# Optimization experiments

Hardware: AMD Instinct MI355X
Metric: run time of the kernel (lower is better)

Reference implementation:

```python
import jax, jax.numpy as jnp
import numpy as np

N_NODES = 10000
N_EDGES = 20000
N_GRAPHS = 64
DIM = 64
NFEAT = 32
EDIM = 16
NCLS = 10
EPS = 1e-5  # BatchNorm eps (torch default)


def setup_inputs() -> dict:
    key = jax.random.key(0)
    ks = jax.random.split(key, 20)
    def w(k, shape, s=0.05):
        return jax.random.normal(k, shape, dtype=jnp.float32) * s
    z = lambda *s: jnp.zeros(s, jnp.float32)
    inp = {}
    inp["x"] = jax.random.normal(ks[0], (N_NODES, NFEAT), dtype=jnp.float32)
    inp["edge_index"] = jax.random.randint(ks[1], (2, N_EDGES), 0, N_NODES)
    inp["edge_attr"] = jax.random.normal(ks[2], (N_EDGES, EDIM), dtype=jnp.float32)
    inp["batch"] = jax.random.randint(ks[3], (N_NODES,), 0, N_GRAPHS)
    # edge_transform
    inp["et_w"] = w(ks[4], (EDIM, DIM)); inp["et_b"] = z(DIM)
    # conv_in edge-MLP (dim->128->num_features*dim) + root weight + bias
    inp["nn1_w1"] = w(ks[5], (DIM, 128)); inp["nn1_b1"] = z(128)
    inp["nn1_w2"] = w(ks[6], (128, NFEAT * DIM)); inp["nn1_b2"] = z(NFEAT * DIM)
    inp["root_in"] = w(ks[7], (NFEAT, DIM)); inp["bias_in"] = z(DIM)
    # 4 residual NNConv layers, params stacked on leading axis
    inp["convs_w1"] = w(ks[8], (4, DIM, 128)); inp["convs_b1"] = z(4, 128)
    inp["convs_w2"] = w(ks[9], (4, 128, DIM * DIM)); inp["convs_b2"] = z(4, DIM * DIM)
    inp["convs_root"] = w(ks[10], (4, DIM, DIM)); inp["convs_bias"] = z(4, DIM)
    # 5 BatchNorm layers (affine)
    inp["bn_gamma"] = jnp.ones((5, DIM), jnp.float32); inp["bn_beta"] = z(5, DIM)
    # head
    inp["lin1_w"] = w(ks[11], (DIM, DIM)); inp["lin1_b"] = z(DIM)
    inp["lin2_w"] = w(ks[12], (DIM, DIM)); inp["lin2_b"] = z(DIM)
    inp["lout_w"] = w(ks[13], (DIM, NCLS)); inp["lout_b"] = z(NCLS)
    return inp


def _bn(x, g, b):
    # BatchNorm1d training-mode math: biased variance over nodes
    m = x.mean(0)
    v = jnp.mean((x - m) ** 2, 0)
    return g * (x - m) / jnp.sqrt(v + EPS) + b


def _nnconv(x, src, dst, e, w1, b1, w2, b2, root, bias, in_dim):
    # PyG NNConv: per-edge weight matrix from edge MLP, gather->bmm->scatter-add, plus root transform
    h = jax.nn.relu(e @ w1 + b1)                       # [E,128]
    W = (h @ w2 + b2).reshape(-1, in_dim, DIM)         # [E,in,out]
    msg = jnp.einsum('ei,eio->eo', x[src], W)          # [E,out]
    agg = jax.ops.segment_sum(msg, dst, num_segments=N_NODES)
    return agg + x @ root + bias


def reference(x, edge_index, edge_attr, batch,
              et_w, et_b,
              nn1_w1, nn1_b1, nn1_w2, nn1_b2, root_in, bias_in,
              convs_w1, convs_b1, convs_w2, convs_b2, convs_root, convs_bias,
              bn_gamma, bn_beta,
              lin1_w, lin1_b, lin2_w, lin2_b, lout_w, lout_b):
    src, dst = edge_index[0], edge_index[1]
    e = edge_attr @ et_w + et_b                        # [E,DIM]
    h = jax.nn.relu(_bn(
        _nnconv(x, src, dst, e, nn1_w1, nn1_b1, nn1_w2, nn1_b2, root_in, bias_in, NFEAT),
        bn_gamma[0], bn_beta[0]))
    for k in range(4):  # residual NNConv blocks
        h = jax.nn.relu(_bn(
            _nnconv(h, src, dst, e, convs_w1[k], convs_b1[k], convs_w2[k], convs_b2[k],
                    convs_root[k], convs_bias[k], DIM),
            bn_gamma[k + 1], bn_beta[k + 1])) + h
    g = jax.ops.segment_max(h, batch, num_segments=N_GRAPHS)  # global_max_pool
    g = jax.nn.relu(g @ lin1_w + lin1_b)  # dropout = identity (eval/deterministic)
    g = jax.nn.relu(g @ lin2_w + lin2_b)
    return jax.nn.sigmoid(g @ lout_w + lout_b)
```

## Files before the change

### kernel.cpp

```cpp
#include <hip/hip_runtime.h>
#include <hip/hip_bf16.h>
#include <math.h>

#define N_NODES 10000
#define N_EDGES 20000
#define EPAD 20224
#define N_GRAPHS 64
#define DIM 64
#define NFEAT 32
#define EDIM 16
#define NCLS 10

typedef short short8 __attribute__((ext_vector_type(8)));
typedef float f32x16 __attribute__((ext_vector_type(16)));

static __device__ __forceinline__ short f2b(float f) {
  __hip_bfloat16 h = __float2bfloat16(f);
  return __builtin_bit_cast(short, h);
}

static __device__ __forceinline__ void gload_lds16(const void* g, void* s) {
  __builtin_amdgcn_global_load_lds(
      (const __attribute__((address_space(1))) unsigned int*)g,
      (__attribute__((address_space(3))) unsigned int*)s, 16, 0, 0);
}

__global__ __launch_bounds__(256) void k_pack_all(
    const float* __restrict__ w20, const float* __restrict__ b20,
    const float* __restrict__ w2c, const float* __restrict__ b2c,
    short* __restrict__ pk, float* __restrict__ gpool) {
  const int b = blockIdx.x, t = threadIdx.x;
  if (b == 0) { for (int i = t; i < N_GRAPHS * DIM; i += 256) gpool[i] = 0.f; }
  __shared__ float tile[32][65];
  const float *w2, *b2; short* out; int K, lb;
  if (b < 129) { w2 = w20; b2 = b20; out = pk; K = 4096; lb = b; }
  else {
    int bb = b - 129; int k = bb / 258; lb = bb % 258;
    w2 = w2c + (size_t)k * 8192 * 64; b2 = b2c + (size_t)k * 4096;
    out = pk + 264192 + (size_t)k * 528384; K = 8192;
  }
  #pragma unroll
  for (int it = 0; it < 2; ++it) {
    int idx = t + it * 256;
    int r = idx >> 4, c4 = idx & 15;
    int k = lb * 32 + r;
    const float* sp = (k < K) ? (w2 + (size_t)k * 64 + c4 * 4)
                              : (b2 + (size_t)(k - K) * 64 + c4 * 4);
    float4 v = *(const float4*)sp;
    float* dr = &tile[r][c4 * 4];
    dr[0] = v.x; dr[1] = v.y; dr[2] = v.z; dr[3] = v.w;
  }
  __syncthreads();
  const int S_local = t >> 7, n = (t >> 6) & 1, l = t & 63;
  const int rbase = S_local * 16 + ((l >> 5) << 3);
  const int col = n * 32 + (l & 31);
  short8 o;
  #pragma unroll
  for (int u = 0; u < 8; ++u) o[u] = f2b(tile[rbase + u][col]);
  ((short8*)out)[(size_t)lb * 256 + t] = o;
}

__global__ __launch_bounds__(256) void k_ef_mlp1(
    const float* __restrict__ ea, const float* __restrict__ etw,
    const float* __restrict__ etb, const float* __restrict__ w1,
    const float* __restrict__ b1, float* __restrict__ e_feat,
    float* __restrict__ h1) {
  __shared__ float sea[8][17];
  __shared__ float se[8][65];
  const int b = blockIdx.x, t = threadIdx.x;
  const int e0 = b * 8;
  if (t < 128) {
    int r = t >> 4, c = t & 15;
    sea[r][c] = ea[(size_t)(e0 + r) * EDIM + c];
  }
  __syncthreads();
  {
    int o = t & 63, eh = t >> 6;
    #pragma unroll
    for (int k = 0; k < 2; ++k) {
      int r = eh * 2 + k;
      float a = etb[o];
      #pragma unroll
      for (int i = 0; i < EDIM; ++i) a = fmaf(sea[r][i], etw[i * 64 + o], a);
      se[r][o] = a;
      e_feat[(size_t)(e0 + r) * 64 + o] = a;
    }
  }
  __syncthreads();
  {
    int j = t & 127, eh = t >> 7;
    int r0 = eh * 4;
    float a0 = b1[j], a1 = a0, a2 = a0, a3 = a0;
    #pragma unroll 8
    for (int i = 0; i < 64; ++i) {
      float wv = w1[i * 128 + j];
      a0 = fmaf(se[r0 + 0][i], wv, a0);
      a1 = fmaf(se[r0 + 1][i], wv, a1);
      a2 = fmaf(se[r0 + 2][i], wv, a2);
      a3 = fmaf(se[r0 + 3][i], wv, a3);
    }
    size_t base = (size_t)(e0 + r0) * 128 + j;
    h1[base +   0] = fmaxf(a0, 0.f);
    h1[base + 128] = fmaxf(a1, 0.f);
    h1[base + 256] = fmaxf(a2, 0.f);
    h1[base + 384] = fmaxf(a3, 0.f);
  }
}

__global__ __launch_bounds__(256) void k_root0(const float* __restrict__ x,
    const float* __restrict__ rootw, const float* __restrict__ rootb,
    float* __restrict__ agg, double* __restrict__ part0) {
  if (blockIdx.x == 0 && threadIdx.x < 128) part0[threadIdx.x] = 0.0;
  int idx = blockIdx.x * 256 + threadIdx.x;
  if (idx >= N_NODES * DIM) return;
  int n = idx >> 6, o = idx & 63;
  float a = rootb[o];
  const float* hr = x + (size_t)n * NFEAT;
  #pragma unroll 8
  for (int i = 0; i < NFEAT; ++i) a = fmaf(hr[i], rootw[i * 64 + o], a);
  agg[idx] = a;
}

template<int IN>
__global__ __launch_bounds__(256, 2) void k_msg(
    const float* __restrict__ h1, const float* __restrict__ xin,
    const int* __restrict__ src, const short* __restrict__ pk,
    float* __restrict__ pt) {
  constexpr int QW = IN / 16;
  constexpr int JR = 32;
  constexpr int GBYTES = QW * 2048;
  __shared__ float sh_h[256][JR + 1];
  __shared__ __align__(16) short bbuf[2][QW * 1024];
  const int t = threadIdx.x, l = t & 63, w = t >> 6;
  const int e0 = blockIdx.x * 256;
  const int jbase = blockIdx.y * JR;
  const int ng = JR + (blockIdx.y == 0 ? 1 : 0);

  const char* pkc = (const char*)pk;
  const char* bias_gb = pkc + (size_t)(8 * IN) * 2048;

  auto stage = [&](int g) {
    const char* gb = (g < JR) ? pkc + (size_t)(jbase + g) * GBYTES : bias_gb;
    #pragma unroll
    for (int s = 0; s < QW / 2; ++s) {
      int off = w * (GBYTES / 4) + s * 1024;
      gload_lds16(gb + off + l * 16, (char*)&bbuf[g & 1][0] + off);
    }
  };

  #pragma unroll
  for (int it = 0; it < 8; ++it) {
    int idx = t + it * 256;
    int row = idx >> 3, c4 = idx & 7;
    int e = e0 + row;
    float4 v = {0.f, 0.f, 0.f, 0.f};
    if (e < N_EDGES) v = *(const float4*)(h1 + (size_t)e * 128 + jbase + c4 * 4);
    float* dr = &sh_h[row][c4 * 4];
    dr[0] = v.x; dr[1] = v.y; dr[2] = v.z; dr[3] = v.w;
  }
  stage(0);

  const int h8 = (l >> 5) << 3;
  float xr[2][QW][8];
  #pragma unroll
  for (int m = 0; m < 2; ++m) {
    int eme = e0 + w * 64 + m * 32 + (l & 31);
    int srow = src[eme < N_EDGES ? eme : 0];
    #pragma unroll
    for (int q = 0; q < QW; ++q) {
      const float* xp = xin + (size_t)srow * IN + q * 16 + h8;
      float4 a = *(const float4*)xp;
      float4 bq = *(const float4*)(xp + 4);
      xr[m][q][0] = a.x;  xr[m][q][1] = a.y;  xr[m][q][2] = a.z;  xr[m][q][3] = a.w;
      xr[m][q][4] = bq.x; xr[m][q][5] = bq.y; xr[m][q][6] = bq.z; xr[m][q][7] = bq.w;
    }
  }

  f32x16 acc00 = {}, acc01 = {}, acc10 = {}, acc11 = {};

  for (int g = 0; g < ng; ++g) {
    asm volatile("s_waitcnt vmcnt(0)" ::: "memory");
    __syncthreads();
    if (g + 1 < ng) stage(g + 1);
    const short8* bp = (const short8*)&bbuf[g & 1][0];
    if (g < JR) {
      float hv0 = sh_h[w * 64 + (l & 31)][g];
      float hv1 = sh_h[w * 64 + 32 + (l & 31)][g];
      #pragma unroll
      for (int q = 0; q < QW; ++q) {
        short8 b0 = bp[q * 128 + l];
        short8 b1 = bp[q * 128 + 64 + l];
        short8 av0, av1;
        #pragma unroll
        for (int u = 0; u < 8; ++u) {
          av0[u] = f2b(hv0 * xr[0][q][u]);
          av1[u] = f2b(hv1 * xr[1][q][u]);
        }
        acc00 = __builtin_amdgcn_mfma_f32_32x32x16_bf16(av0, b0, acc00, 0, 0, 0);
        acc01 = __builtin_amdgcn_mfma_f32_32x32x16_bf16(av0, b1, acc01, 0, 0, 0);
        acc10 = __builtin_amdgcn_mfma_f32_32x32x16_bf16(av1, b0, acc10, 0, 0, 0);
        acc11 = __builtin_amdgcn_mfma_f32_32x32x16_bf16(av1, b1, acc11, 0, 0, 0);
      }
    } else {
      #pragma unroll
      for (int q = 0; q < QW; ++q) {
        short8 b0 = bp[q * 128 + l];
        short8 b1 = bp[q * 128 + 64 + l];
        short8 av0, av1;
        #pragma unroll
        for (int u = 0; u < 8; ++u) {
          av0[u] = f2b(xr[0][q][u]);
          av1[u] = f2b(xr[1][q][u]);
        }
        acc00 = __builtin_amdgcn_mfma_f32_32x32x16_bf16(av0, b0, acc00, 0, 0, 0);
        acc01 = __builtin_amdgcn_mfma_f32_32x32x16_bf16(av0, b1, acc01, 0, 0, 0);
        acc10 = __builtin_amdgcn_mfma_f32_32x32x16_bf16(av1, b0, acc10, 0, 0, 0);
        acc11 = __builtin_amdgcn_mfma_f32_32x32x16_bf16(av1, b1, acc11, 0, 0, 0);
      }
    }
  }

  float* po = pt + ((size_t)blockIdx.y * EPAD + e0 + w * 64) * 64 + (l & 31);
  #pragma unroll
  for (int v = 0; v < 16; ++v) {
    int r = (v & 3) + ((v >> 2) << 3) + ((l >> 5) << 2);
    po[(size_t)r * 64]             = acc00[v];
    po[(size_t)r * 64 + 32]       = acc01[v];
    po[(size_t)(r + 32) * 64]      = acc10[v];
    po[(size_t)(r + 32) * 64 + 32] = acc11[v];
  }
}

__global__ __launch_bounds__(256) void k_reduce(const float* __restrict__ pt,
    const int* __restrict__ dst, float* __restrict__ agg) {
  int idx = blockIdx.x * 256 + threadIdx.x;
  int e = idx >> 4;
  if (e >= N_EDGES) return;
  int c = (idx & 15) * 4;
  const float* p = pt + (size_t)e * 64 + c;
  float4 s0 = *(const float4*)p;
  float4 s1 = *(const float4*)(p + (size_t)EPAD * 64);
  float4 s2 = *(const float4*)(p + (size_t)2 * EPAD * 64);
  float4 s3 = *(const float4*)(p + (size_t)3 * EPAD * 64);
  float* ap = agg + (size_t)dst[e] * 64 + c;
  atomicAdd(ap + 0, s0.x + s1.x + s2.x + s3.x);
  atomicAdd(ap + 1, s0.y + s1.y + s2.y + s3.y);
  atomicAdd(ap + 2, s0.z + s1.z + s2.z + s3.z);
  atomicAdd(ap + 3, s0.w + s1.w + s2.w + s3.w);
}

__global__ __launch_bounds__(256) void k_bnpart(const float* __restrict__ agg,
    double* __restrict__ part) {
  const int t = threadIdx.x;
  const int c = t & 63, rg = t >> 6;
  const int r0 = blockIdx.x * 50;
  const int r1 = min(r0 + 50, N_NODES);
  double s = 0.0, s2 = 0.0;
  for (int r = r0 + rg; r < r1; r += 4) {
    float v = agg[(size_t)r * 64 + c];
    s += v;
    s2 += (double)v * v;
  }
  __shared__ double shs[4][64];
  __shared__ double shq[4][64];
  shs[rg][c] = s; shq[rg][c] = s2;
  __syncthreads();
  if (t < 64) {
    double ts = shs[0][t] + shs[1][t] + shs[2][t] + shs[3][t];
    double tq = shq[0][t] + shq[1][t] + shq[2][t] + shq[3][t];
    atomicAdd(&part[t], ts);
    atomicAdd(&part[64 + t], tq);
  }
}

__global__ __launch_bounds__(256) void k_inter(
    const float* __restrict__ agg, const double* __restrict__ part,
    const float* __restrict__ gamma, const float* __restrict__ beta,
    const float* resid, float* __restrict__ hout,
    const float* __restrict__ rootw, const float* __restrict__ rootb,
    float* __restrict__ aggn, double* __restrict__ partn,
    const float* __restrict__ ef, const float* __restrict__ w1,
    const float* __restrict__ b1, float* __restrict__ h1) {
  const int b = blockIdx.x, t = threadIdx.x;
  if (b < 157) {
    __shared__ float sh[64][65];
    if (b == 0 && t < 128) partn[t] = 0.0;
    const int o = t & 63, rg = t >> 6;
    const int n0 = b * 64;
    float m = (float)(part[o] * (1.0 / N_NODES));
    float s2 = (float)(part[64 + o] * (1.0 / N_NODES));
    float inv = 1.0f / sqrtf(s2 - m * m + 1e-5f);
    float sc = gamma[o] * inv;
    float sf = beta[o] - m * sc;
    #pragma unroll
    for (int k = 0; k < 16; ++k) {
      int r = rg * 16 + k;
      int n = n0 + r;
      float v = 0.f;
      if (n < N_NODES) {
        v = fmaxf(fmaf(agg[(size_t)n * 64 + o], sc, sf), 0.f);
        if (resid) v += resid[(size_t)n * 64 + o];
        hout[(size_t)n * 64 + o] = v;
      }
      sh[r][o] = v;
    }
    __syncthreads();
    float acc[16];
    float rb = rootb[o];
    #pragma unroll
    for (int k = 0; k < 16; ++k) acc[k] = rb;
    for (int i = 0; i < 64; ++i) {
      float wv = rootw[i * 64 + o];
      #pragma unroll
      for (int k = 0; k < 16; ++k) acc[k] = fmaf(sh[rg * 16 + k][i], wv, acc[k]);
    }
    #pragma unroll
    for (int k = 0; k < 16; ++k) {
      int n = n0 + rg * 16 + k;
      if (n < N_NODES) aggn[(size_t)n * 64 + o] = acc[k];
    }
  } else {
    const int e0 = (b - 157) * 8;
    __shared__ float se[8][65];
    {
      int r = t >> 5, ci = (t & 31) * 2;
      const float* sp = ef + (size_t)(e0 + r) * 64 + ci;
      se[r][ci] = sp[0];
      se[r][ci + 1] = sp[1];
    }
    __syncthreads();
    const int j = t & 127, eh = t >> 7;
    const int r0 = eh * 4;
    float a0 = b1[j], a1 = a0, a2 = a0, a3 = a0;
    #pragma unroll 8
    for (int i = 0; i < 64; ++i) {
      float wv = w1[i * 128 + j];
      a0 = fmaf(se[r0 + 0][i], wv, a0);
      a1 = fmaf(se[r0 + 1][i], wv, a1);
      a2 = fmaf(se[r0 + 2][i], wv, a2);
      a3 = fmaf(se[r0 + 3][i], wv, a3);
    }
    size_t base = (size_t)(e0 + r0) * 128 + j;
    h1[base +   0] = fmaxf(a0, 0.f);
    h1[base + 128] = fmaxf(a1, 0.f);
    h1[base + 256] = fmaxf(a2, 0.f);
    h1[base + 384] = fmaxf(a3, 0.f);
  }
}

__global__ __launch_bounds__(256) void k_final(const float* __restrict__ agg,
    const double* __restrict__ part, const float* __restrict__ gamma,
    const float* __restrict__ beta, const float* __restrict__ resid,
    const int* __restrict__ batch, float* __restrict__ gpool) {
  int idx = blockIdx.x * 256 + threadIdx.x;
  if (idx >= N_NODES * DIM) return;
  int c = idx & 63, r = idx >> 6;
  float m = (float)(part[c] * (1.0 / N_NODES));
  float s2 = (float)(part[64 + c] * (1.0 / N_NODES));
  float inv = 1.0f / sqrtf(s2 - m * m + 1e-5f);
  float sc = gamma[c] * inv;
  float sf = beta[c] - m * sc;
  float v = fmaxf(fmaf(agg[idx], sc, sf), 0.f) + resid[idx];
  atomicMax((unsigned int*)&gpool[batch[r] * 64 + c], __float_as_uint(v));
}

__global__ __launch_bounds__(64) void k_head(const float* __restrict__ g,
    const float* __restrict__ w1, const float* __restrict__ b1,
    const float* __restrict__ w2, const float* __restrict__ b2,
    const float* __restrict__ wo, const float* __restrict__ bo,
    float* __restrict__ out) {
  __shared__ float s0[64];
  __shared__ float s1[64];
  const int r = blockIdx.x, t = threadIdx.x;
  s0[t] = g[r * 64 + t];
  __syncthreads();
  float a = b1[t];
  #pragma unroll 8
  for (int i = 0; i < 64; ++i) a = fmaf(s0[i], w1[i * 64 + t], a);
  s1[t] = fmaxf(a, 0.f);
  __syncthreads();
  a = b2[t];
  #pragma unroll 8
  for (int i = 0; i < 64; ++i) a = fmaf(s1[i], w2[i * 64 + t], a);
  __syncthreads();
  s0[t] = fmaxf(a, 0.f);
  __syncthreads();
  if (t < NCLS) {
    float o = bo[t];
    #pragma unroll 8
    for (int i = 0; i < 64; ++i) o = fmaf(s0[i], wo[i * NCLS + t], o);
    out[r * NCLS + t] = 1.f / (1.f + expf(-o));
  }
}

extern "C" void kernel_launch(void* const* d_in, const int* in_sizes, int n_in,
                              void* d_out, int out_size, void* d_ws, size_t ws_size,
                              hipStream_t stream) {
  const float* x          = (const float*)d_in[0];
  const int*   eidx       = (const int*)d_in[1];
  const float* eattr      = (const float*)d_in[2];
  const int*   batch      = (const int*)d_in[3];
  const float* et_w       = (const float*)d_in[4];
  const float* et_b       = (const float*)d_in[5];
  const float* nn1_w1     = (const float*)d_in[6];
  const float* nn1_b1     = (const float*)d_in[7];
  const float* nn1_w2     = (const float*)d_in[8];
  const float* nn1_b2     = (const float*)d_in[9];
  const float* root_in    = (const float*)d_in[10];
  const float* bias_in    = (const float*)d_in[11];
  const float* convs_w1   = (const float*)d_in[12];
  const float* convs_b1   = (const float*)d_in[13];
  const float* convs_w2   = (const float*)d_in[14];
  const float* convs_b2   = (const float*)d_in[15];
  const float* convs_root = (const float*)d_in[16];
  const float* convs_bias = (const float*)d_in[17];
  const float* bn_gamma   = (const float*)d_in[18];
  const float* bn_beta    = (const float*)d_in[19];
  const float* lin1_w     = (const float*)d_in[20];
  const float* lin1_b     = (const float*)d_in[21];
  const float* lin2_w     = (const float*)d_in[22];
  const float* lin2_b     = (const float*)d_in[23];
  const float* lout_w     = (const float*)d_in[24];
  const float* lout_b     = (const float*)d_in[25];

  const int* srcp = eidx;
  const int* dstp = eidx + N_EDGES;

  double* part0 = (double*)d_ws;
  double* part1 = part0 + 128;
  float* e_feat = (float*)(part0 + 256);
  float* h1     = e_feat + N_EDGES * DIM;
  float* agg    = h1 + N_EDGES * 128;
  float* h_cur  = agg + N_NODES * DIM;
  float* g      = h_cur + N_NODES * DIM;
  short* pk0    = (short*)(g + N_GRAPHS * DIM);
  short* pkL[4];
  for (int k = 0; k < 4; ++k) pkL[k] = pk0 + 264192 + (size_t)k * 528384;
  float* pt     = (float*)(pk0 + 264192 + 4 * 528384);
  double* parts[2] = {part0, part1};

  const dim3 gMsg(79, 4);
  const int gRed = EPAD * 16 / 256;

  k_pack_all<<<1161, 256, 0, stream>>>(nn1_w2, nn1_b2, convs_w2, convs_b2, pk0, g);
  k_ef_mlp1<<<2500, 256, 0, stream>>>(eattr, et_w, et_b, nn1_w1, nn1_b1,
                                      e_feat, h1);
  k_root0<<<2500, 256, 0, stream>>>(x, root_in, bias_in, agg, part0);

  k_msg<NFEAT><<<gMsg, 256, 0, stream>>>(h1, x, srcp, pk0, pt);
  k_reduce<<<gRed, 256, 0, stream>>>(pt, dstp, agg);
  k_bnpart<<<200, 256, 0, stream>>>(agg, part0);

  for (int k = 0; k < 4; ++k) {
    k_inter<<<2657, 256, 0, stream>>>(
        agg, parts[k & 1], bn_gamma + k * 64, bn_beta + k * 64,
        (k == 0) ? nullptr : h_cur, h_cur,
        convs_root + (size_t)k * 4096, convs_bias + (size_t)k * 64,
        agg, parts[(k + 1) & 1],
        e_feat, convs_w1 + (size_t)k * 64 * 128, convs_b1 + (size_t)k * 128, h1);
    k_msg<DIM><<<gMsg, 256, 0, stream>>>(h1, h_cur, srcp, pkL[k], pt);
    k_reduce<<<gRed, 256, 0, stream>>>(pt, dstp, agg);
    k_bnpart<<<200, 256, 0, stream>>>(agg, parts[(k + 1) & 1]);
  }

  k_final<<<2500, 256, 0, stream>>>(agg, parts[0], bn_gamma + 4 * 64,
                                    bn_beta + 4 * 64, h_cur, batch, g);
  k_head<<<N_GRAPHS, 64, 0, stream>>>(g, lin1_w, lin1_b, lin2_w, lin2_b,
                                      lout_w, lout_b, (float*)d_out);
}
```

Measured before the change: 444.6 us.

## Fuse edge reduction into message kernel and split hidden units across waves

The message kernel is restructured so that each block owns 64 edges and its four waves split the 128 hidden units, 32 each. Weight fragments are now read straight from global memory into registers with double buffering, replacing the LDS staging. The per-wave partial results are summed in LDS and scattered to nodes with atomics inside the same kernel. This removes the separate reduce kernel and the large partial-sum buffer, and the edge-MLP output is stored transposed so per-edge hidden values load coalesced. In exchange, every block re-reads the whole packed weight matrix from global or L2 memory instead of sharing a staged copy, and register pressure rises.

```diff
diff --git a/kernel.cpp b/kernel.cpp
--- a/kernel.cpp
+++ b/kernel.cpp
@@ -17,12 +17,6 @@
 static __device__ __forceinline__ short f2b(float f) {
   __hip_bfloat16 h = __float2bfloat16(f);
   return __builtin_bit_cast(short, h);
-}
-
-static __device__ __forceinline__ void gload_lds16(const void* g, void* s) {
-  __builtin_amdgcn_global_load_lds(
-      (const __attribute__((address_space(1))) unsigned int*)g,
-      (__attribute__((address_space(3))) unsigned int*)s, 16, 0, 0);
 }
 
 __global__ __launch_bounds__(256) void k_pack_all(
@@ -64,7 +58,7 @@
     const float* __restrict__ ea, const float* __restrict__ etw,
     const float* __restrict__ etb, const float* __restrict__ w1,
     const float* __restrict__ b1, float* __restrict__ e_feat,
-    float* __restrict__ h1) {
+    float* __restrict__ h1T) {
   __shared__ float sea[8][17];
   __shared__ float se[8][65];
   const int b = blockIdx.x, t = threadIdx.x;
@@ -99,11 +93,8 @@
       a2 = fmaf(se[r0 + 2][i], wv, a2);
       a3 = fmaf(se[r0 + 3][i], wv, a3);
     }
-    size_t base = (size_t)(e0 + r0) * 128 + j;
-    h1[base +   0] = fmaxf(a0, 0.f);
-    h1[base + 128] = fmaxf(a1, 0.f);
-    h1[base + 256] = fmaxf(a2, 0.f);
-    h1[base + 384] = fmaxf(a3, 0.f);
+    float4 o = {fmaxf(a0, 0.f), fmaxf(a1, 0.f), fmaxf(a2, 0.f), fmaxf(a3, 0.f)};
+    *(float4*)(h1T + (size_t)j * EPAD + e0 + r0) = o;
   }
 }
 
@@ -123,48 +114,23 @@
 
 template<int IN>
 __global__ __launch_bounds__(256, 2) void k_msg(
-    const float* __restrict__ h1, const float* __restrict__ xin,
-    const int* __restrict__ src, const short* __restrict__ pk,
-    float* __restrict__ pt) {
+    const float* __restrict__ h1T, const float* __restrict__ xin,
+    const int* __restrict__ src, const int* __restrict__ dst,
+    const short* __restrict__ pk, float* __restrict__ agg) {
   constexpr int QW = IN / 16;
   constexpr int JR = 32;
-  constexpr int GBYTES = QW * 2048;
-  __shared__ float sh_h[256][JR + 1];
-  __shared__ __align__(16) short bbuf[2][QW * 1024];
+  __shared__ float red[4][64][68];
   const int t = threadIdx.x, l = t & 63, w = t >> 6;
-  const int e0 = blockIdx.x * 256;
-  const int jbase = blockIdx.y * JR;
-  const int ng = JR + (blockIdx.y == 0 ? 1 : 0);
-
-  const char* pkc = (const char*)pk;
-  const char* bias_gb = pkc + (size_t)(8 * IN) * 2048;
-
-  auto stage = [&](int g) {
-    const char* gb = (g < JR) ? pkc + (size_t)(jbase + g) * GBYTES : bias_gb;
-    #pragma unroll
-    for (int s = 0; s < QW / 2; ++s) {
-      int off = w * (GBYTES / 4) + s * 1024;
-      gload_lds16(gb + off + l * 16, (char*)&bbuf[g & 1][0] + off);
-    }
-  };
-
-  #pragma unroll
-  for (int it = 0; it < 8; ++it) {
-    int idx = t + it * 256;
-    int row = idx >> 3, c4 = idx & 7;
-    int e = e0 + row;
-    float4 v = {0.f, 0.f, 0.f, 0.f};
-    if (e < N_EDGES) v = *(const float4*)(h1 + (size_t)e * 128 + jbase + c4 * 4);
-    float* dr = &sh_h[row][c4 * 4];
-    dr[0] = v.x; dr[1] = v.y; dr[2] = v.z; dr[3] = v.w;
-  }
-  stage(0);
-
+  const int e0 = blockIdx.x * 64;
+  const int jbase = w * JR;
+  const int col = l & 31;
   const int h8 = (l >> 5) << 3;
+  const short8* B = (const short8*)pk;
+
   float xr[2][QW][8];
   #pragma unroll
   for (int m = 0; m < 2; ++m) {
-    int eme = e0 + w * 64 + m * 32 + (l & 31);
+    int eme = e0 + m * 32 + col;
     int srow = src[eme < N_EDGES ? eme : 0];
     #pragma unroll
     for (int q = 0; q < QW; ++q) {
@@ -178,75 +144,87 @@
 
   f32x16 acc00 = {}, acc01 = {}, acc10 = {}, acc11 = {};
 
-  for (int g = 0; g < ng; ++g) {
-    asm volatile("s_waitcnt vmcnt(0)" ::: "memory");
-    __syncthreads();
-    if (g + 1 < ng) stage(g + 1);
-    const short8* bp = (const short8*)&bbuf[g & 1][0];
-    if (g < JR) {
-      float hv0 = sh_h[w * 64 + (l & 31)][g];
-      float hv1 = sh_h[w * 64 + 32 + (l & 31)][g];
+  short8 bufA[QW * 2], bufB[QW * 2];
+  float2 hA, hB;
+
+#define LOADB(buf, j)                                              \
+  { int S0_ = (j) * QW;                                            \
+    _Pragma("unroll")                                              \
+    for (int q = 0; q < QW; ++q) {                                 \
+      buf[q * 2]     = B[(size_t)(S0_ + q) * 128 + l];             \
+      buf[q * 2 + 1] = B[(size_t)(S0_ + q) * 128 + 64 + l];        \
+    } }
+#define LOADH(hv, j)                                               \
+  { hv.x = h1T[(size_t)(j) * EPAD + e0 + col];                     \
+    hv.y = h1T[(size_t)(j) * EPAD + e0 + 32 + col]; }
+#define COMPUTE(buf, hv)                                           \
+  { _Pragma("unroll")                                              \
+    for (int q = 0; q < QW; ++q) {                                 \
+      short8 av0, av1;                                             \
+      _Pragma("unroll")                                            \
+      for (int u = 0; u < 8; ++u) {                                \
+        av0[u] = f2b(hv.x * xr[0][q][u]);                          \
+        av1[u] = f2b(hv.y * xr[1][q][u]);                          \
+      }                                                            \
+      acc00 = __builtin_amdgcn_mfma_f32_32x32x16_bf16(av0, buf[q*2],   acc00, 0, 0, 0); \
+      acc01 = __builtin_amdgcn_mfma_f32_32x32x16_bf16(av0, buf[q*2+1], acc01, 0, 0, 0); \
+      acc10 = __builtin_amdgcn_mfma_f32_32x32x16_bf16(av1, buf[q*2],   acc10, 0, 0, 0); \
+      acc11 = __builtin_amdgcn_mfma_f32_32x32x16_bf16(av1, buf[q*2+1], acc11, 0, 0, 0); \
+    } }
+
+  LOADB(bufA, jbase); LOADH(hA, jbase);
+  for (int g = 0; g < JR; g += 2) {
+    LOADB(bufB, jbase + g + 1); LOADH(hB, jbase + g + 1);
+    COMPUTE(bufA, hA);
+    if (g + 2 < JR) { LOADB(bufA, jbase + g + 2); LOADH(hA, jbase + g + 2); }
+    COMPUTE(bufB, hB);
+  }
+  if (w == 0) {
+    LOADB(bufA, 128);
+    #pragma unroll
+    for (int q = 0; q < QW; ++q) {
+      short8 av0, av1;
       #pragma unroll
-      for (int q = 0; q < QW; ++q) {
-        short8 b0 = bp[q * 128 + l];
-        short8 b1 = bp[q * 128 + 64 + l];
-        short8 av0, av1;
-        #pragma unroll
-        for (int u = 0; u < 8; ++u) {
-          av0[u] = f2b(hv0 * xr[0][q][u]);
-          av1[u] = f2b(hv1 * xr[1][q][u]);
-        }
-        acc00 = __builtin_amdgcn_mfma_f32_32x32x16_bf16(av0, b0, acc00, 0, 0, 0);
-        acc01 = __builtin_amdgcn_mfma_f32_32x32x16_bf16(av0, b1, acc01, 0, 0, 0);
-        acc10 = __builtin_amdgcn_mfma_f32_32x32x16_bf16(av1, b0, acc10, 0, 0, 0);
-        acc11 = __builtin_amdgcn_mfma_f32_32x32x16_bf16(av1, b1, acc11, 0, 0, 0);
+      for (int u = 0; u < 8; ++u) {
+        av0[u] = f2b(xr[0][q][u]);
+        av1[u] = f2b(xr[1][q][u]);
       }
-    } else {
-      #pragma unroll
-      for (int q = 0; q < QW; ++q) {
-        short8 b0 = bp[q * 128 + l];
-        short8 b1 = bp[q * 128 + 64 + l];
-        short8 av0, av1;
-        #pragma unroll
-        for (int u = 0; u < 8; ++u) {
-          av0[u] = f2b(xr[0][q][u]);
-          av1[u] = f2b(xr[1][q][u]);
-        }
-        acc00 = __builtin_amdgcn_mfma_f32_32x32x16_bf16(av0, b0, acc00, 0, 0, 0);
-        acc01 = __builtin_amdgcn_mfma_f32_32x32x16_bf16(av0, b1, acc01, 0, 0, 0);
-        acc10 = __builtin_amdgcn_mfma_f32_32x32x16_bf16(av1, b0, acc10, 0, 0, 0);
-        acc11 = __builtin_amdgcn_mfma_f32_32x32x16_bf16(av1, b1, acc11, 0, 0, 0);
-      }
-    }
-  }
-
-  float* po = pt + ((size_t)blockIdx.y * EPAD + e0 + w * 64) * 64 + (l & 31);
+      acc00 = __builtin_amdgcn_mfma_f32_32x32x16_bf16(av0, bufA[q*2],   acc00, 0, 0, 0);
+      acc01 = __builtin_amdgcn_mfma_f32_32x32x16_bf16(av0, bufA[q*2+1], acc01, 0, 0, 0);
+      acc10 = __builtin_amdgcn_mfma_f32_32x32x16_bf16(av1, bufA[q*2],   acc10, 0, 0, 0);
+      acc11 = __builtin_amdgcn_mfma_f32_32x32x16_bf16(av1, bufA[q*2+1], acc11, 0, 0, 0);
+    }
+  }
+#undef LOADB
+#undef LOADH
+#undef COMPUTE
+
   #pragma unroll
   for (int v = 0; v < 16; ++v) {
     int r = (v & 3) + ((v >> 2) << 3) + ((l >> 5) << 2);
-    po[(size_t)r * 64]             = acc00[v];
-    po[(size_t)r * 64 + 32]       = acc01[v];
-    po[(size_t)(r + 32) * 64]      = acc10[v];
-    po[(size_t)(r + 32) * 64 + 32] = acc11[v];
-  }
-}
-
-__global__ __launch_bounds__(256) void k_reduce(const float* __restrict__ pt,
-    const int* __restrict__ dst, float* __restrict__ agg) {
-  int idx = blockIdx.x * 256 + threadIdx.x;
-  int e = idx >> 4;
-  if (e >= N_EDGES) return;
-  int c = (idx & 15) * 4;
-  const float* p = pt + (size_t)e * 64 + c;
-  float4 s0 = *(const float4*)p;
-  float4 s1 = *(const float4*)(p + (size_t)EPAD * 64);
-  float4 s2 = *(const float4*)(p + (size_t)2 * EPAD * 64);
-  float4 s3 = *(const float4*)(p + (size_t)3 * EPAD * 64);
-  float* ap = agg + (size_t)dst[e] * 64 + c;
-  atomicAdd(ap + 0, s0.x + s1.x + s2.x + s3.x);
-  atomicAdd(ap + 1, s0.y + s1.y + s2.y + s3.y);
-  atomicAdd(ap + 2, s0.z + s1.z + s2.z + s3.z);
-  atomicAdd(ap + 3, s0.w + s1.w + s2.w + s3.w);
+    red[w][r][col]           = acc00[v];
+    red[w][r][col + 32]      = acc01[v];
+    red[w][r + 32][col]      = acc10[v];
+    red[w][r + 32][col + 32] = acc11[v];
+  }
+  __syncthreads();
+
+  const int row = t >> 2, cq = (t & 3) * 16;
+  const int e = e0 + row;
+  if (e < N_EDGES) {
+    float* ap = agg + (size_t)dst[e] * 64 + cq;
+    #pragma unroll
+    for (int cc = 0; cc < 4; ++cc) {
+      float4 s0 = *(const float4*)&red[0][row][cq + cc * 4];
+      float4 s1 = *(const float4*)&red[1][row][cq + cc * 4];
+      float4 s2 = *(const float4*)&red[2][row][cq + cc * 4];
+      float4 s3 = *(const float4*)&red[3][row][cq + cc * 4];
+      atomicAdd(ap + cc * 4 + 0, s0.x + s1.x + s2.x + s3.x);
+      atomicAdd(ap + cc * 4 + 1, s0.y + s1.y + s2.y + s3.y);
+      atomicAdd(ap + cc * 4 + 2, s0.z + s1.z + s2.z + s3.z);
+      atomicAdd(ap + cc * 4 + 3, s0.w + s1.w + s2.w + s3.w);
+    }
+  }
 }
 
 __global__ __launch_bounds__(256) void k_bnpart(const float* __restrict__ agg,
@@ -280,7 +258,7 @@
     const float* __restrict__ rootw, const float* __restrict__ rootb,
     float* __restrict__ aggn, double* __restrict__ partn,
     const float* __restrict__ ef, const float* __restrict__ w1,
-    const float* __restrict__ b1, float* __restrict__ h1) {
+    const float* __restrict__ b1, float* __restrict__ h1T) {
   const int b = blockIdx.x, t = threadIdx.x;
   if (b < 157) {
     __shared__ float sh[64][65];
@@ -340,11 +318,8 @@
       a2 = fmaf(se[r0 + 2][i], wv, a2);
       a3 = fmaf(se[r0 + 3][i], wv, a3);
     }
-    size_t base = (size_t)(e0 + r0) * 128 + j;
-    h1[base +   0] = fmaxf(a0, 0.f);
-    h1[base + 128] = fmaxf(a1, 0.f);
-    h1[base + 256] = fmaxf(a2, 0.f);
-    h1[base + 384] = fmaxf(a3, 0.f);
+    float4 o = {fmaxf(a0, 0.f), fmaxf(a1, 0.f), fmaxf(a2, 0.f), fmaxf(a3, 0.f)};
+    *(float4*)(h1T + (size_t)j * EPAD + e0 + r0) = o;
   }
 }
 
@@ -429,26 +404,23 @@
   double* part0 = (double*)d_ws;
   double* part1 = part0 + 128;
   float* e_feat = (float*)(part0 + 256);
-  float* h1     = e_feat + N_EDGES * DIM;
-  float* agg    = h1 + N_EDGES * 128;
+  float* h1T    = e_feat + N_EDGES * DIM;
+  float* agg    = h1T + 128 * EPAD;
   float* h_cur  = agg + N_NODES * DIM;
   float* g      = h_cur + N_NODES * DIM;
   short* pk0    = (short*)(g + N_GRAPHS * DIM);
   short* pkL[4];
   for (int k = 0; k < 4; ++k) pkL[k] = pk0 + 264192 + (size_t)k * 528384;
-  float* pt     = (float*)(pk0 + 264192 + 4 * 528384);
   double* parts[2] = {part0, part1};
 
-  const dim3 gMsg(79, 4);
-  const int gRed = EPAD * 16 / 256;
+  const int gMsg = (N_EDGES + 63) / 64;
 
   k_pack_all<<<1161, 256, 0, stream>>>(nn1_w2, nn1_b2, convs_w2, convs_b2, pk0, g);
   k_ef_mlp1<<<2500, 256, 0, stream>>>(eattr, et_w, et_b, nn1_w1, nn1_b1,
-                                      e_feat, h1);
+                                      e_feat, h1T);
   k_root0<<<2500, 256, 0, stream>>>(x, root_in, bias_in, agg, part0);
 
-  k_msg<NFEAT><<<gMsg, 256, 0, stream>>>(h1, x, srcp, pk0, pt);
-  k_reduce<<<gRed, 256, 0, stream>>>(pt, dstp, agg);
+  k_msg<NFEAT><<<gMsg, 256, 0, stream>>>(h1T, x, srcp, dstp, pk0, agg);
   k_bnpart<<<200, 256, 0, stream>>>(agg, part0);
 
   for (int k = 0; k < 4; ++k) {
@@ -457,9 +429,8 @@
         (k == 0) ? nullptr : h_cur, h_cur,
         convs_root + (size_t)k * 4096, convs_bias + (size_t)k * 64,
         agg, parts[(k + 1) & 1],
-        e_feat, convs_w1 + (size_t)k * 64 * 128, convs_b1 + (size_t)k * 128, h1);
-    k_msg<DIM><<<gMsg, 256, 0, stream>>>(h1, h_cur, srcp, pkL[k], pt);
-    k_reduce<<<gRed, 256, 0, stream>>>(pt, dstp, agg);
+        e_feat, convs_w1 + (size_t)k * 64 * 128, convs_b1 + (size_t)k * 128, h1T);
+    k_msg<DIM><<<gMsg, 256, 0, stream>>>(h1T, h_cur, srcp, dstp, pkL[k], agg);
     k_bnpart<<<200, 256, 0, stream>>>(agg, parts[(k + 1) & 1]);
   }
 
```

Result: slower. 684.1 us (+53.9%).

## Fuse prologue kernels, transpose h1, triple-buffer weight staging, split msg into 8 chunks

Applied to the files above, without the earlier changes.

Merges the pack, edge-MLP and root kernels into one launch. Stores the hidden edge features transposed (h1T) so k_msg loads them with coalesced float4 reads. The grid's j-dimension grows from 4 to 8 chunks to raise parallelism, and weight staging moves to a three-deep LDS buffer with partial vmcnt waits. The per-layer edge features are now recomputed from edge_attr instead of being stored, and k_reduce sums 8 partials instead of 4, which doubles partial-buffer traffic.

```diff
diff --git a/kernel.cpp b/kernel.cpp
--- a/kernel.cpp
+++ b/kernel.cpp
@@ -11,6 +11,8 @@
 #define EDIM 16
 #define NCLS 10
 
+static_assert(EPAD == 79 * 256, "EPAD");
+
 typedef short short8 __attribute__((ext_vector_type(8)));
 typedef float f32x16 __attribute__((ext_vector_type(16)));
 
@@ -25,112 +27,107 @@
       (__attribute__((address_space(3))) unsigned int*)s, 16, 0, 0);
 }
 
-__global__ __launch_bounds__(256) void k_pack_all(
+__global__ __launch_bounds__(256) void k_pre(
+    const float* __restrict__ ea, const float* __restrict__ etw,
+    const float* __restrict__ etb, const float* __restrict__ nw1,
+    const float* __restrict__ nb1, const float* __restrict__ x,
+    const float* __restrict__ rootw, const float* __restrict__ rootb,
     const float* __restrict__ w20, const float* __restrict__ b20,
     const float* __restrict__ w2c, const float* __restrict__ b2c,
-    short* __restrict__ pk, float* __restrict__ gpool) {
+    float* __restrict__ h1T, float* __restrict__ agg,
+    double* __restrict__ part0, short* __restrict__ pk,
+    float* __restrict__ gpool) {
   const int b = blockIdx.x, t = threadIdx.x;
-  if (b == 0) { for (int i = t; i < N_GRAPHS * DIM; i += 256) gpool[i] = 0.f; }
-  __shared__ float tile[32][65];
-  const float *w2, *b2; short* out; int K, lb;
-  if (b < 129) { w2 = w20; b2 = b20; out = pk; K = 4096; lb = b; }
-  else {
-    int bb = b - 129; int k = bb / 258; lb = bb % 258;
-    w2 = w2c + (size_t)k * 8192 * 64; b2 = b2c + (size_t)k * 4096;
-    out = pk + 264192 + (size_t)k * 528384; K = 8192;
-  }
-  #pragma unroll
-  for (int it = 0; it < 2; ++it) {
-    int idx = t + it * 256;
-    int r = idx >> 4, c4 = idx & 15;
-    int k = lb * 32 + r;
-    const float* sp = (k < K) ? (w2 + (size_t)k * 64 + c4 * 4)
-                              : (b2 + (size_t)(k - K) * 64 + c4 * 4);
-    float4 v = *(const float4*)sp;
-    float* dr = &tile[r][c4 * 4];
-    dr[0] = v.x; dr[1] = v.y; dr[2] = v.z; dr[3] = v.w;
-  }
-  __syncthreads();
-  const int S_local = t >> 7, n = (t >> 6) & 1, l = t & 63;
-  const int rbase = S_local * 16 + ((l >> 5) << 3);
-  const int col = n * 32 + (l & 31);
-  short8 o;
-  #pragma unroll
-  for (int u = 0; u < 8; ++u) o[u] = f2b(tile[rbase + u][col]);
-  ((short8*)out)[(size_t)lb * 256 + t] = o;
-}
-
-__global__ __launch_bounds__(256) void k_ef_mlp1(
-    const float* __restrict__ ea, const float* __restrict__ etw,
-    const float* __restrict__ etb, const float* __restrict__ w1,
-    const float* __restrict__ b1, float* __restrict__ e_feat,
-    float* __restrict__ h1) {
-  __shared__ float sea[8][17];
-  __shared__ float se[8][65];
-  const int b = blockIdx.x, t = threadIdx.x;
-  const int e0 = b * 8;
-  if (t < 128) {
-    int r = t >> 4, c = t & 15;
-    sea[r][c] = ea[(size_t)(e0 + r) * EDIM + c];
-  }
-  __syncthreads();
-  {
-    int o = t & 63, eh = t >> 6;
-    #pragma unroll
-    for (int k = 0; k < 2; ++k) {
-      int r = eh * 2 + k;
-      float a = etb[o];
+  if (b < 1161) {
+    if (b == 0) { for (int i = t; i < N_GRAPHS * DIM; i += 256) gpool[i] = 0.f; }
+    __shared__ float tile[32][65];
+    const float *w2, *b2; short* out; int K, lb;
+    if (b < 129) { w2 = w20; b2 = b20; out = pk; K = 4096; lb = b; }
+    else {
+      int bb = b - 129; int k = bb / 258; lb = bb % 258;
+      w2 = w2c + (size_t)k * 8192 * 64; b2 = b2c + (size_t)k * 4096;
+      out = pk + 264192 + (size_t)k * 528384; K = 8192;
+    }
+    #pragma unroll
+    for (int it = 0; it < 2; ++it) {
+      int idx = t + it * 256;
+      int r = idx >> 4, c4 = idx & 15;
+      int k = lb * 32 + r;
+      const float* sp = (k < K) ? (w2 + (size_t)k * 64 + c4 * 4)
+                                : (b2 + (size_t)(k - K) * 64 + c4 * 4);
+      float4 v = *(const float4*)sp;
+      float* dr = &tile[r][c4 * 4];
+      dr[0] = v.x; dr[1] = v.y; dr[2] = v.z; dr[3] = v.w;
+    }
+    __syncthreads();
+    const int S_local = t >> 7, n = (t >> 6) & 1, l = t & 63;
+    const int rbase = S_local * 16 + ((l >> 5) << 3);
+    const int col = n * 32 + (l & 31);
+    short8 o;
+    #pragma unroll
+    for (int u = 0; u < 8; ++u) o[u] = f2b(tile[rbase + u][col]);
+    ((short8*)out)[(size_t)lb * 256 + t] = o;
+  } else if (b < 3661) {
+    const int e0 = (b - 1161) * 8;
+    __shared__ float sea[8][17];
+    __shared__ float se[8][65];
+    if (t < 128) {
+      int r = t >> 4, c = t & 15;
+      sea[r][c] = ea[(size_t)(e0 + r) * EDIM + c];
+    }
+    __syncthreads();
+    {
+      int o = t & 63, eh = t >> 6;
       #pragma unroll
-      for (int i = 0; i < EDIM; ++i) a = fmaf(sea[r][i], etw[i * 64 + o], a);
-      se[r][o] = a;
-      e_feat[(size_t)(e0 + r) * 64 + o] = a;
-    }
-  }
-  __syncthreads();
-  {
-    int j = t & 127, eh = t >> 7;
-    int r0 = eh * 4;
-    float a0 = b1[j], a1 = a0, a2 = a0, a3 = a0;
-    #pragma unroll 8
-    for (int i = 0; i < 64; ++i) {
-      float wv = w1[i * 128 + j];
-      a0 = fmaf(se[r0 + 0][i], wv, a0);
-      a1 = fmaf(se[r0 + 1][i], wv, a1);
-      a2 = fmaf(se[r0 + 2][i], wv, a2);
-      a3 = fmaf(se[r0 + 3][i], wv, a3);
-    }
-    size_t base = (size_t)(e0 + r0) * 128 + j;
-    h1[base +   0] = fmaxf(a0, 0.f);
-    h1[base + 128] = fmaxf(a1, 0.f);
-    h1[base + 256] = fmaxf(a2, 0.f);
-    h1[base + 384] = fmaxf(a3, 0.f);
-  }
-}
-
-__global__ __launch_bounds__(256) void k_root0(const float* __restrict__ x,
-    const float* __restrict__ rootw, const float* __restrict__ rootb,
-    float* __restrict__ agg, double* __restrict__ part0) {
-  if (blockIdx.x == 0 && threadIdx.x < 128) part0[threadIdx.x] = 0.0;
-  int idx = blockIdx.x * 256 + threadIdx.x;
-  if (idx >= N_NODES * DIM) return;
-  int n = idx >> 6, o = idx & 63;
-  float a = rootb[o];
-  const float* hr = x + (size_t)n * NFEAT;
-  #pragma unroll 8
-  for (int i = 0; i < NFEAT; ++i) a = fmaf(hr[i], rootw[i * 64 + o], a);
-  agg[idx] = a;
-}
-
-template<int IN>
+      for (int k = 0; k < 2; ++k) {
+        int r = eh * 2 + k;
+        float a = etb[o];
+        #pragma unroll
+        for (int i = 0; i < EDIM; ++i) a = fmaf(sea[r][i], etw[i * 64 + o], a);
+        se[r][o] = a;
+      }
+    }
+    __syncthreads();
+    {
+      int j = t & 127, eh = t >> 7;
+      int r0 = eh * 4;
+      float a0 = nb1[j], a1 = a0, a2 = a0, a3 = a0;
+      #pragma unroll 8
+      for (int i = 0; i < 64; ++i) {
+        float wv = nw1[i * 128 + j];
+        a0 = fmaf(se[r0 + 0][i], wv, a0);
+        a1 = fmaf(se[r0 + 1][i], wv, a1);
+        a2 = fmaf(se[r0 + 2][i], wv, a2);
+        a3 = fmaf(se[r0 + 3][i], wv, a3);
+      }
+      float4 o = {fmaxf(a0, 0.f), fmaxf(a1, 0.f), fmaxf(a2, 0.f), fmaxf(a3, 0.f)};
+      *(float4*)(h1T + (size_t)j * EPAD + e0 + r0) = o;
+    }
+  } else {
+    const int u = b - 3661;
+    if (u == 0 && t < 128) part0[t] = 0.0;
+    int idx = u * 256 + t;
+    if (idx < N_NODES * DIM) {
+      int n = idx >> 6, o = idx & 63;
+      float a = rootb[o];
+      const float* hr = x + (size_t)n * NFEAT;
+      #pragma unroll 8
+      for (int i = 0; i < NFEAT; ++i) a = fmaf(hr[i], rootw[i * 64 + o], a);
+      agg[idx] = a;
+    }
+  }
+}
+
+template<int IN, int NC>
 __global__ __launch_bounds__(256, 2) void k_msg(
-    const float* __restrict__ h1, const float* __restrict__ xin,
+    const float* __restrict__ h1T, const float* __restrict__ xin,
     const int* __restrict__ src, const short* __restrict__ pk,
     float* __restrict__ pt) {
   constexpr int QW = IN / 16;
-  constexpr int JR = 32;
-  constexpr int GBYTES = QW * 2048;
+  constexpr int JR = 128 / NC;
+  constexpr int GB = QW * 2048;
   __shared__ float sh_h[256][JR + 1];
-  __shared__ __align__(16) short bbuf[2][QW * 1024];
+  __shared__ __align__(16) short bbuf[3][QW * 1024];
   const int t = threadIdx.x, l = t & 63, w = t >> 6;
   const int e0 = blockIdx.x * 256;
   const int jbase = blockIdx.y * JR;
@@ -140,25 +137,24 @@
   const char* bias_gb = pkc + (size_t)(8 * IN) * 2048;
 
   auto stage = [&](int g) {
-    const char* gb = (g < JR) ? pkc + (size_t)(jbase + g) * GBYTES : bias_gb;
+    const char* gb = (g < JR) ? pkc + (size_t)(jbase + g) * GB : bias_gb;
     #pragma unroll
     for (int s = 0; s < QW / 2; ++s) {
-      int off = w * (GBYTES / 4) + s * 1024;
-      gload_lds16(gb + off + l * 16, (char*)&bbuf[g & 1][0] + off);
+      int off = w * (QW * 512) + s * 1024;
+      gload_lds16(gb + off + l * 16, (char*)&bbuf[g % 3][0] + off);
     }
   };
 
   #pragma unroll
-  for (int it = 0; it < 8; ++it) {
-    int idx = t + it * 256;
-    int row = idx >> 3, c4 = idx & 7;
-    int e = e0 + row;
-    float4 v = {0.f, 0.f, 0.f, 0.f};
-    if (e < N_EDGES) v = *(const float4*)(h1 + (size_t)e * 128 + jbase + c4 * 4);
-    float* dr = &sh_h[row][c4 * 4];
-    dr[0] = v.x; dr[1] = v.y; dr[2] = v.z; dr[3] = v.w;
-  }
-  stage(0);
+  for (int it = 0; it < JR / 4; ++it) {
+    int u = t + it * 256;
+    int jj = u >> 6, c4 = u & 63;
+    float4 v = *(const float4*)(h1T + (size_t)(jbase + jj) * EPAD + e0 + c4 * 4);
+    sh_h[c4 * 4 + 0][jj] = v.x;
+    sh_h[c4 * 4 + 1][jj] = v.y;
+    sh_h[c4 * 4 + 2][jj] = v.z;
+    sh_h[c4 * 4 + 3][jj] = v.w;
+  }
 
   const int h8 = (l >> 5) << 3;
   float xr[2][QW][8];
@@ -176,13 +172,22 @@
     }
   }
 
+  asm volatile("s_waitcnt vmcnt(0) lgkmcnt(0)" ::: "memory");
+  stage(0);
+  if (ng > 1) stage(1);
+
   f32x16 acc00 = {}, acc01 = {}, acc10 = {}, acc11 = {};
 
   for (int g = 0; g < ng; ++g) {
-    asm volatile("s_waitcnt vmcnt(0)" ::: "memory");
-    __syncthreads();
-    if (g + 1 < ng) stage(g + 1);
-    const short8* bp = (const short8*)&bbuf[g & 1][0];
+    if (g + 1 < ng) {
+      if constexpr (QW / 2 == 2) asm volatile("s_waitcnt vmcnt(2)" ::: "memory");
+      else                       asm volatile("s_waitcnt vmcnt(1)" ::: "memory");
+    } else {
+      asm volatile("s_waitcnt vmcnt(0)" ::: "memory");
+    }
+    asm volatile("s_barrier" ::: "memory");
+    if (g + 2 < ng) stage(g + 2);
+    const short8* bp = (const short8*)&bbuf[g % 3][0];
     if (g < JR) {
       float hv0 = sh_h[w * 64 + (l & 31)][g];
       float hv1 = sh_h[w * 64 + 32 + (l & 31)][g];
@@ -225,7 +230,7 @@
   for (int v = 0; v < 16; ++v) {
     int r = (v & 3) + ((v >> 2) << 3) + ((l >> 5) << 2);
     po[(size_t)r * 64]             = acc00[v];
-    po[(size_t)r * 64 + 32]       = acc01[v];
+    po[(size_t)r * 64 + 32]        = acc01[v];
     po[(size_t)(r + 32) * 64]      = acc10[v];
     po[(size_t)(r + 32) * 64 + 32] = acc11[v];
   }
@@ -236,17 +241,19 @@
   int idx = blockIdx.x * 256 + threadIdx.x;
   int e = idx >> 4;
   if (e >= N_EDGES) return;
-  int c = (idx & 15) * 4;
+  int c = (idx & 15) << 2;
   const float* p = pt + (size_t)e * 64 + c;
-  float4 s0 = *(const float4*)p;
-  float4 s1 = *(const float4*)(p + (size_t)EPAD * 64);
-  float4 s2 = *(const float4*)(p + (size_t)2 * EPAD * 64);
-  float4 s3 = *(const float4*)(p + (size_t)3 * EPAD * 64);
+  float4 a = *(const float4*)p;
+  #pragma unroll
+  for (int s = 1; s < 8; ++s) {
+    float4 b = *(const float4*)(p + (size_t)s * EPAD * 64);
+    a.x += b.x; a.y += b.y; a.z += b.z; a.w += b.w;
+  }
   float* ap = agg + (size_t)dst[e] * 64 + c;
-  atomicAdd(ap + 0, s0.x + s1.x + s2.x + s3.x);
-  atomicAdd(ap + 1, s0.y + s1.y + s2.y + s3.y);
-  atomicAdd(ap + 2, s0.z + s1.z + s2.z + s3.z);
-  atomicAdd(ap + 3, s0.w + s1.w + s2.w + s3.w);
+  atomicAdd(ap + 0, a.x);
+  atomicAdd(ap + 1, a.y);
+  atomicAdd(ap + 2, a.z);
+  atomicAdd(ap + 3, a.w);
 }
 
 __global__ __launch_bounds__(256) void k_bnpart(const float* __restrict__ agg,
@@ -274,13 +281,14 @@
 }
 
 __global__ __launch_bounds__(256) void k_inter(
-    const float* __restrict__ agg, const double* __restrict__ part,
+    float* __restrict__ agg, const double* __restrict__ part,
     const float* __restrict__ gamma, const float* __restrict__ beta,
-    const float* resid, float* __restrict__ hout,
+    const float* resid, float* __restrict__ h_cur,
     const float* __restrict__ rootw, const float* __restrict__ rootb,
-    float* __restrict__ aggn, double* __restrict__ partn,
-    const float* __restrict__ ef, const float* __restrict__ w1,
-    const float* __restrict__ b1, float* __restrict__ h1) {
+    double* __restrict__ partn,
+    const float* __restrict__ ea, const float* __restrict__ etw,
+    const float* __restrict__ etb, const float* __restrict__ w1,
+    const float* __restrict__ b1, float* __restrict__ h1T) {
   const int b = blockIdx.x, t = threadIdx.x;
   if (b < 157) {
     __shared__ float sh[64][65];
@@ -300,7 +308,7 @@
       if (n < N_NODES) {
         v = fmaxf(fmaf(agg[(size_t)n * 64 + o], sc, sf), 0.f);
         if (resid) v += resid[(size_t)n * 64 + o];
-        hout[(size_t)n * 64 + o] = v;
+        h_cur[(size_t)n * 64 + o] = v;
       }
       sh[r][o] = v;
     }
@@ -317,34 +325,44 @@
     #pragma unroll
     for (int k = 0; k < 16; ++k) {
       int n = n0 + rg * 16 + k;
-      if (n < N_NODES) aggn[(size_t)n * 64 + o] = acc[k];
+      if (n < N_NODES) agg[(size_t)n * 64 + o] = acc[k];
     }
   } else {
     const int e0 = (b - 157) * 8;
+    __shared__ float sea[8][17];
     __shared__ float se[8][65];
+    if (t < 128) {
+      int r = t >> 4, c = t & 15;
+      sea[r][c] = ea[(size_t)(e0 + r) * EDIM + c];
+    }
+    __syncthreads();
     {
-      int r = t >> 5, ci = (t & 31) * 2;
-      const float* sp = ef + (size_t)(e0 + r) * 64 + ci;
-      se[r][ci] = sp[0];
-      se[r][ci + 1] = sp[1];
-    }
-    __syncthreads();
-    const int j = t & 127, eh = t >> 7;
-    const int r0 = eh * 4;
-    float a0 = b1[j], a1 = a0, a2 = a0, a3 = a0;
-    #pragma unroll 8
-    for (int i = 0; i < 64; ++i) {
-      float wv = w1[i * 128 + j];
-      a0 = fmaf(se[r0 + 0][i], wv, a0);
-      a1 = fmaf(se[r0 + 1][i], wv, a1);
-      a2 = fmaf(se[r0 + 2][i], wv, a2);
-      a3 = fmaf(se[r0 + 3][i], wv, a3);
-    }
-    size_t base = (size_t)(e0 + r0) * 128 + j;
-    h1[base +   0] = fmaxf(a0, 0.f);
-    h1[base + 128] = fmaxf(a1, 0.f);
-    h1[base + 256] = fmaxf(a2, 0.f);
-    h1[base + 384] = fmaxf(a3, 0.f);
+      int o = t & 63, eh = t >> 6;
+      #pragma unroll
+      for (int k = 0; k < 2; ++k) {
+        int r = eh * 2 + k;
+        float a = etb[o];
+        #pragma unroll
+        for (int i = 0; i < EDIM; ++i) a = fmaf(sea[r][i], etw[i * 64 + o], a);
+        se[r][o] = a;
+      }
+    }
+    __syncthreads();
+    {
+      int j = t & 127, eh = t >> 7;
+      int r0 = eh * 4;
+      float a0 = b1[j], a1 = a0, a2 = a0, a3 = a0;
+      #pragma unroll 8
+      for (int i = 0; i < 64; ++i) {
+        float wv = w1[i * 128 + j];
+        a0 = fmaf(se[r0 + 0][i], wv, a0);
+        a1 = fmaf(se[r0 + 1][i], wv, a1);
+        a2 = fmaf(se[r0 + 2][i], wv, a2);
+        a3 = fmaf(se[r0 + 3][i], wv, a3);
+      }
+      float4 o = {fmaxf(a0, 0.f), fmaxf(a1, 0.f), fmaxf(a2, 0.f), fmaxf(a3, 0.f)};
+      *(float4*)(h1T + (size_t)j * EPAD + e0 + r0) = o;
+    }
   }
 }
 
@@ -426,29 +444,25 @@
   const int* srcp = eidx;
   const int* dstp = eidx + N_EDGES;
 
-  double* part0 = (double*)d_ws;
-  double* part1 = part0 + 128;
-  float* e_feat = (float*)(part0 + 256);
-  float* h1     = e_feat + N_EDGES * DIM;
-  float* agg    = h1 + N_EDGES * 128;
-  float* h_cur  = agg + N_NODES * DIM;
-  float* g      = h_cur + N_NODES * DIM;
-  short* pk0    = (short*)(g + N_GRAPHS * DIM);
+  char* wsb = (char*)d_ws;
+  double* part0 = (double*)wsb;
+  double* part1 = (double*)(wsb + 1024);
+  float* h1T    = (float*)(wsb + 4096);
+  float* agg    = h1T + 128 * EPAD;
+  float* h_cur  = agg + N_NODES * 64;
+  float* g      = h_cur + N_NODES * 64;
+  short* pk0    = (short*)(g + N_GRAPHS * 64);
   short* pkL[4];
   for (int k = 0; k < 4; ++k) pkL[k] = pk0 + 264192 + (size_t)k * 528384;
   float* pt     = (float*)(pk0 + 264192 + 4 * 528384);
   double* parts[2] = {part0, part1};
 
-  const dim3 gMsg(79, 4);
-  const int gRed = EPAD * 16 / 256;
-
-  k_pack_all<<<1161, 256, 0, stream>>>(nn1_w2, nn1_b2, convs_w2, convs_b2, pk0, g);
-  k_ef_mlp1<<<2500, 256, 0, stream>>>(eattr, et_w, et_b, nn1_w1, nn1_b1,
-                                      e_feat, h1);
-  k_root0<<<2500, 256, 0, stream>>>(x, root_in, bias_in, agg, part0);
-
-  k_msg<NFEAT><<<gMsg, 256, 0, stream>>>(h1, x, srcp, pk0, pt);
-  k_reduce<<<gRed, 256, 0, stream>>>(pt, dstp, agg);
+  k_pre<<<6161, 256, 0, stream>>>(eattr, et_w, et_b, nn1_w1, nn1_b1, x,
+                                  root_in, bias_in, nn1_w2, nn1_b2,
+                                  convs_w2, convs_b2, h1T, agg, part0, pk0, g);
+
+  k_msg<32, 8><<<dim3(79, 8), 256, 0, stream>>>(h1T, x, srcp, pk0, pt);
+  k_reduce<<<(EPAD * 16) / 256, 256, 0, stream>>>(pt, dstp, agg);
   k_bnpart<<<200, 256, 0, stream>>>(agg, part0);
 
   for (int k = 0; k < 4; ++k) {
@@ -456,10 +470,11 @@
         agg, parts[k & 1], bn_gamma + k * 64, bn_beta + k * 64,
         (k == 0) ? nullptr : h_cur, h_cur,
         convs_root + (size_t)k * 4096, convs_bias + (size_t)k * 64,
-        agg, parts[(k + 1) & 1],
-        e_feat, convs_w1 + (size_t)k * 64 * 128, convs_b1 + (size_t)k * 128, h1);
-    k_msg<DIM><<<gMsg, 256, 0, stream>>>(h1, h_cur, srcp, pkL[k], pt);
-    k_reduce<<<gRed, 256, 0, stream>>>(pt, dstp, agg);
+        parts[(k + 1) & 1],
+        eattr, et_w, et_b,
+        convs_w1 + (size_t)k * 8192, convs_b1 + (size_t)k * 128, h1T);
+    k_msg<64, 8><<<dim3(79, 8), 256, 0, stream>>>(h1T, h_cur, srcp, pkL[k], pt);
+    k_reduce<<<(EPAD * 16) / 256, 256, 0, stream>>>(pt, dstp, agg);
     k_bnpart<<<200, 256, 0, stream>>>(agg, parts[(k + 1) & 1]);
   }
 
```

Result: no change. 449.7 us (+1.1%).
